# Optimization experiments

Hardware: AMD Instinct MI355X
Metric: run time of the kernel (lower is better)

The kernel has to match this reference:

```python
import jax, jax.numpy as jnp
import numpy as np
from jax import lax

N_KERNELS = 10000
IN_CH = 3
BATCH = 64
T_LEN = 1024
KSIZES = [7, 9, 11]
DILS = [1, 2, 4, 8, 16]
MAXK = max(KSIZES)

# Deterministic stand-in for torch's random per-kernel (size, dilation) draw.
_rng = np.random.default_rng(0)
_ks = np.array(KSIZES)[_rng.integers(0, len(KSIZES), N_KERNELS)]
_dil = np.array(DILS)[_rng.integers(0, len(DILS), N_KERNELS)]
GROUPS = []  # (kernel_size, dilation, static index array)
for _k in KSIZES:
    for _d in DILS:
        _idx = np.nonzero((_ks == _k) & (_dil == _d))[0]
        if _idx.size:
            GROUPS.append((_k, _d, _idx))
_PERM = np.concatenate([g[2] for g in GROUPS])  # grouped order -> original kernel id
INV_PERM = np.argsort(_PERM)                    # restore original kernel order


def setup_inputs() -> dict:
    key = jax.random.key(0)
    kx, kw, kb = jax.random.split(key, 3)
    x = jax.random.normal(kx, (BATCH, IN_CH, T_LEN), dtype=jnp.float32)
    # Weights padded to MAXK taps; taps beyond each kernel's size are zeroed
    # (zero taps do not change the conv output within the valid window).
    w = jax.random.normal(kw, (N_KERNELS, IN_CH, MAXK), dtype=jnp.float32)
    tap_mask = (np.arange(MAXK)[None, :] < _ks[:, None]).astype(np.float32)
    weights = w * jnp.asarray(tap_mask)[:, None, :]
    biases = 0.1 * jax.random.normal(kb, (N_KERNELS,), dtype=jnp.float32)
    return {"x": x, "weights": weights, "biases": biases}


def _rocket(x, weights, biases):
    # Group kernels by (size, dilation) -> <=15 batched convs instead of 10000 tiny ones.
    maxs, ppvs = [], []
    for k, d, idx in GROUPS:
        w = weights[idx, :, :k]                 # (G, C, k), idx is a static np array
        pad = (k - 1) * d // 2                  # 'same' padding (k odd -> exact)
        out = lax.conv_general_dilated(
            x, w, window_strides=(1,), padding=[(pad, pad)],
            rhs_dilation=(d,), dimension_numbers=("NCH", "OIH", "NCH"))
        out = out + biases[idx][None, :, None]  # (B, G, T)
        maxs.append(out.max(-1))                             # max pooling feature
        ppvs.append((out > 0).astype(jnp.float32).mean(-1))  # PPV feature
    mx = jnp.concatenate(maxs, 1)[:, INV_PERM]  # (B, N) in original kernel order
    pv = jnp.concatenate(ppvs, 1)[:, INV_PERM]
    # Interleave [max_0, ppv_0, max_1, ppv_1, ...] like torch.stack(features, dim=1)
    return jnp.stack([mx, pv], -1).reshape(x.shape[0], 2 * N_KERNELS)


def reference(x, weights, biases):
    return _rocket(x, weights, biases)
```

## Files before the change

### kernel.cpp

```cpp
#include <hip/hip_runtime.h>
#include <stdint.h>

#define N_KERNELS 10000
#define NCHUNK 56
#define CH_ALLOC 1312
#define PP_STRIDE (3 * CH_ALLOC)
#define NPHASE 4

typedef unsigned __int128 u128;
typedef __attribute__((ext_vector_type(4)))  short short4v;
typedef __attribute__((ext_vector_type(8)))  short short8;
typedef __attribute__((ext_vector_type(16))) float floatx16;

struct KDraws { uint8_t k[N_KERNELS]; uint8_t d[N_KERNELS]; };

constexpr KDraws make_kd() {
    KDraws kd{};
    const u128 MULT = (((u128)0x2360ED051FC65DA4ULL) << 64) | 0x4385DF649FCCF645ULL;

    uint32_t hc = 0x43b0d7e5u;
    uint32_t pool[4] = {};
    for (int i = 0; i < 4; i++) {
        uint32_t v = 0u;
        v ^= hc; hc *= 0x931e8875u;
        v *= hc; v ^= v >> 16;
        pool[i] = v;
    }
    for (int s = 0; s < 4; s++)
        for (int dd = 0; dd < 4; dd++)
            if (s != dd) {
                uint32_t hv = pool[s];
                hv ^= hc; hc *= 0x931e8875u;
                hv *= hc; hv ^= hv >> 16;
                uint32_t rr = 0xca01f9ddu * pool[dd] - 0x4973f715u * hv;
                rr ^= rr >> 16;
                pool[dd] = rr;
            }
    uint32_t st[8] = {};
    uint32_t hcb = 0x8b51f9ddu;
    for (int i = 0; i < 8; i++) {
        uint32_t dv = pool[i & 3];
        dv ^= hcb; hcb *= 0x58f38dedu;
        dv *= hcb; dv ^= dv >> 16;
        st[i] = dv;
    }
    uint64_t w0 = (uint64_t)st[0] | ((uint64_t)st[1] << 32);
    uint64_t w1 = (uint64_t)st[2] | ((uint64_t)st[3] << 32);
    uint64_t w2 = (uint64_t)st[4] | ((uint64_t)st[5] << 32);
    uint64_t w3 = (uint64_t)st[6] | ((uint64_t)st[7] << 32);
    u128 initstate = (((u128)w0) << 64) | w1;
    u128 initseq   = (((u128)w2) << 64) | w3;

    u128 inc   = (initseq << 1) | 1;
    u128 state = 0;
    state = state * MULT + inc;
    state += initstate;
    state = state * MULT + inc;

    u128 s = state;
    for (int t = 0; t < 10000; ++t) {
        s = s * MULT + inc;
        uint64_t hi = (uint64_t)(s >> 64), lo = (uint64_t)s;
        unsigned rot = (unsigned)(hi >> 58);
        uint64_t v = hi ^ lo;
        uint64_t o = (v >> rot) | (v << ((64u - rot) & 63u));
        uint32_t d0 = (uint32_t)o;
        uint32_t d1 = (uint32_t)(o >> 32);
        int i0 = 2 * t, i1 = 2 * t + 1;
        if (i0 < 10000) kd.k[i0] = (uint8_t)(((uint64_t)d0 * 3u) >> 32);
        else            kd.d[i0 - 10000] = (uint8_t)(((uint64_t)d0 * 5u) >> 32);
        if (i1 < 10000) kd.k[i1] = (uint8_t)(((uint64_t)d1 * 3u) >> 32);
        else            kd.d[i1 - 10000] = (uint8_t)(((uint64_t)d1 * 5u) >> 32);
    }
    return kd;
}

constexpr KDraws kdr = make_kd();

struct Tables {
    alignas(16) int sched[4 * NCHUNK];
    int list[N_KERNELS];
};

constexpr Tables make_tables(const KDraws& kd) {
    Tables T{};
    int cnt[15] = {}, off[15] = {}, cur[15] = {};
    for (int i = 0; i < 10000; ++i) cnt[(int)kd.k[i] * 5 + (int)kd.d[i]]++;
    int o = 0;
    for (int g = 0; g < 15; ++g) { off[g] = o; cur[g] = o; o += cnt[g]; }
    for (int i = 0; i < 10000; ++i) {
        int g = (int)kd.k[i] * 5 + (int)kd.d[i];
        T.list[cur[g]++] = i;
    }
    const int kv[3] = {7, 9, 11};
    int ci = 0;
    for (int g = 0; g < 15; ++g) {
        int sz = cnt[g];
        for (int s2 = 0; s2 < sz; s2 += 256) {
            T.sched[4 * ci + 0] = kv[g / 5];
            T.sched[4 * ci + 1] = g % 5;
            T.sched[4 * ci + 2] = off[g] + s2;
            T.sched[4 * ci + 3] = (sz - s2 < 256) ? (sz - s2) : 256;
            ci++;
        }
    }
    for (; ci < NCHUNK; ci++) {
        T.sched[4 * ci + 0] = 0; T.sched[4 * ci + 1] = 0;
        T.sched[4 * ci + 2] = 0; T.sched[4 * ci + 3] = 0;
    }
    return T;
}

__constant__ Tables g_T = make_tables(kdr);

__device__ __forceinline__ uint16_t f32_to_bf16(float v) {
    uint32_t u = __builtin_bit_cast(uint32_t, v);
    return (uint16_t)((u + 0x7FFFu + ((u >> 16) & 1u)) >> 16);
}

__device__ __forceinline__ void stat16(const floatx16& C, float& mx, int& cnt) {
    float g0 = fmaxf(fmaxf(C[0],  C[1]),  C[2]);
    float g1 = fmaxf(fmaxf(C[3],  C[4]),  C[5]);
    float g2 = fmaxf(fmaxf(C[6],  C[7]),  C[8]);
    float g3 = fmaxf(fmaxf(C[9],  C[10]), C[11]);
    float g4 = fmaxf(fmaxf(C[12], C[13]), C[14]);
    float h0 = fmaxf(fmaxf(g0, g1), g2);
    float h1 = fmaxf(fmaxf(g3, g4), C[15]);
    mx = fmaxf(mx, fmaxf(h0, h1));
    #pragma unroll
    for (int i = 0; i < 16; i += 2) {
        int s0 = __builtin_bit_cast(int, C[i])     >> 31;
        int s1 = __builtin_bit_cast(int, C[i + 1]) >> 31;
        cnt += s0 + s1;
    }
}

__device__ __forceinline__ int swz_g(int g) { return g ^ ((g >> 4) & 3); }

template <int K, int D>
__device__ __forceinline__ void body(const float* __restrict__ x,
                                     const float* __restrict__ wgt,
                                     const float* __restrict__ bias,
                                     int lstart, int valid,
                                     float* __restrict__ out,
                                     short* __restrict__ xs,
                                     int b) {
    constexpr int H   = (K - 1) / 2;
    constexpr int Q   = 1024 / D;
    constexpr int S   = Q + 16;
    constexpr int RS  = (D <= 4) ? 8 : (D == 8 ? 4 : 2);
    constexpr int NIT = 32;

    const int tid   = threadIdx.x;
    const int lane  = tid & 63;
    const int wave  = tid >> 6;
    const int jbase = (lane >> 5) * 8;
    const int m31   = lane & 31;

    for (int idx = tid; idx < 3 * (CH_ALLOC + NPHASE); idx += 256) {
        int c = idx / (CH_ALLOC + NPHASE);
        int P = idx - c * (CH_ALLOC + NPHASE);
        float v = 0.f;
        int y = P - 8;
        if (y >= 0) {
            int r = y / S;
            int q = y - r * S;
            if (r < D && q < Q) v = x[((size_t)b * 3 + c) * 1024 + r + D * q];
        }
        short hv = (short)f32_to_bf16(v);
        #pragma unroll
        for (int pp = 0; pp < NPHASE; ++pp) {
            int ee = P - pp;
            if (ee >= 0 && ee < CH_ALLOC) {
                int phys = (swz_g(ee >> 2) << 2) | (ee & 3);
                xs[pp * PP_STRIDE + c * CH_ALLOC + phys] = hv;
            }
        }
    }

    int i0 = wave * 64 + m31;
    int i1 = i0 + 32;
    int n0 = g_T.list[lstart + (i0 < valid ? i0 : valid - 1)];
    int n1 = g_T.list[lstart + (i1 < valid ? i1 : valid - 1)];
    short8 whi[2][3];
    #pragma unroll
    for (int t2 = 0; t2 < 2; ++t2) {
        int n = t2 ? n1 : n0;
        #pragma unroll
        for (int c = 0; c < 3; ++c) {
            #pragma unroll
            for (int u = 0; u < 8; ++u) {
                int j = jbase + u;
                float wv = (j < 11) ? wgt[n * 33 + c * 11 + j] : 0.f;
                whi[t2][c][u] = (short)f32_to_bf16(wv);
            }
        }
    }
    float bv0 = bias[n0], bv1 = bias[n1];

    floatx16 BT0, BT1;
    #pragma unroll
    for (int i = 0; i < 16; ++i) { BT0[i] = bv0; BT1[i] = bv1; }

    __syncthreads();

    auto calcF = [&](int it) -> int {
        int ri, p;
        if (D <= 4)      { ri = it >> 3; p = it & 7; }
        else if (D == 8) { ri = it >> 2; p = it & 3; }
        else             { ri = it >> 1; p = it & 1; }
        int q0;
        if (D == 1)      q0 = 8 + ri * 256;
        else if (D == 2) q0 = 8 + (ri >> 1) * S + (ri & 1) * 256;
        else             q0 = 8 + ri * S;
        return q0 + p - H + RS * m31;
    };
    auto loadfrag = [&](int F, short8& A0, short8& A1, short8& A2) {
        int g0 = (F >> 2) + (jbase >> 2);
        int s0 = swz_g(g0) << 2;
        int s1 = swz_g(g0 + 1) << 2;
        const short* bp = xs + (F & 3) * PP_STRIDE;
        short4v l0 = *reinterpret_cast<const short4v*>(bp + s0);
        short4v h0 = *reinterpret_cast<const short4v*>(bp + s1);
        short4v l1 = *reinterpret_cast<const short4v*>(bp + CH_ALLOC + s0);
        short4v h1 = *reinterpret_cast<const short4v*>(bp + CH_ALLOC + s1);
        short4v l2 = *reinterpret_cast<const short4v*>(bp + 2 * CH_ALLOC + s0);
        short4v h2 = *reinterpret_cast<const short4v*>(bp + 2 * CH_ALLOC + s1);
        A0 = __builtin_shufflevector(l0, h0, 0, 1, 2, 3, 4, 5, 6, 7);
        A1 = __builtin_shufflevector(l1, h1, 0, 1, 2, 3, 4, 5, 6, 7);
        A2 = __builtin_shufflevector(l2, h2, 0, 1, 2, 3, 4, 5, 6, 7);
    };

    float mx0 = -3.402823466e38f, mx1 = -3.402823466e38f;
    int cnt0 = 0, cnt1 = 0;

    short8 a0, a1, a2, b0, b1, b2;
    loadfrag(calcF(0), a0, a1, a2);
    loadfrag(calcF(1), b0, b1, b2);

    #pragma unroll 1
    for (int it = 0; it < NIT; it += 2) {
        int itA = (it + 2 < NIT) ? it + 2 : NIT - 1;
        int itB = (it + 3 < NIT) ? it + 3 : NIT - 1;

        floatx16 C0, C1;
        C0 = __builtin_amdgcn_mfma_f32_32x32x16_bf16(a0, whi[0][0], BT0, 0, 0, 0);
        C0 = __builtin_amdgcn_mfma_f32_32x32x16_bf16(a1, whi[0][1], C0, 0, 0, 0);
        C0 = __builtin_amdgcn_mfma_f32_32x32x16_bf16(a2, whi[0][2], C0, 0, 0, 0);
        C1 = __builtin_amdgcn_mfma_f32_32x32x16_bf16(a0, whi[1][0], BT1, 0, 0, 0);
        C1 = __builtin_amdgcn_mfma_f32_32x32x16_bf16(a1, whi[1][1], C1, 0, 0, 0);
        C1 = __builtin_amdgcn_mfma_f32_32x32x16_bf16(a2, whi[1][2], C1, 0, 0, 0);
        loadfrag(calcF(itA), a0, a1, a2);
        stat16(C0, mx0, cnt0);
        stat16(C1, mx1, cnt1);

        floatx16 D0, D1;
        D0 = __builtin_amdgcn_mfma_f32_32x32x16_bf16(b0, whi[0][0], BT0, 0, 0, 0);
        D0 = __builtin_amdgcn_mfma_f32_32x32x16_bf16(b1, whi[0][1], D0, 0, 0, 0);
        D0 = __builtin_amdgcn_mfma_f32_32x32x16_bf16(b2, whi[0][2], D0, 0, 0, 0);
        D1 = __builtin_amdgcn_mfma_f32_32x32x16_bf16(b0, whi[1][0], BT1, 0, 0, 0);
        D1 = __builtin_amdgcn_mfma_f32_32x32x16_bf16(b1, whi[1][1], D1, 0, 0, 0);
        D1 = __builtin_amdgcn_mfma_f32_32x32x16_bf16(b2, whi[1][2], D1, 0, 0, 0);
        loadfrag(calcF(itB), b0, b1, b2);
        stat16(D0, mx0, cnt0);
        stat16(D1, mx1, cnt1);
    }

    mx0  = fmaxf(mx0, __shfl_xor(mx0, 32));
    mx1  = fmaxf(mx1, __shfl_xor(mx1, 32));
    cnt0 += __shfl_xor(cnt0, 32);
    cnt1 += __shfl_xor(cnt1, 32);

    if (lane < 32) {
        float2* ob = reinterpret_cast<float2*>(out + (size_t)b * (2 * N_KERNELS));
        ob[n0] = make_float2(mx0, (float)(1024 + cnt0) * (1.0f / 1024.0f));
        ob[n1] = make_float2(mx1, (float)(1024 + cnt1) * (1.0f / 1024.0f));
    }
}

__global__ __launch_bounds__(256, 4)
void rocket_main(const float* __restrict__ x, const float* __restrict__ wgt,
                 const float* __restrict__ bias, float* __restrict__ out) {
    __shared__ __align__(16) short xs[NPHASE * PP_STRIDE];
    int kc     = g_T.sched[4 * blockIdx.x + 0];
    int ld2    = g_T.sched[4 * blockIdx.x + 1];
    int lstart = g_T.sched[4 * blockIdx.x + 2];
    int valid  = g_T.sched[4 * blockIdx.x + 3];
    if (valid == 0) return;
    int b = blockIdx.y;
    switch (kc * 8 + ld2) {
        case 7*8+0:  body<7, 1 >(x, wgt, bias, lstart, valid, out, xs, b); break;
        case 7*8+1:  body<7, 2 >(x, wgt, bias, lstart, valid, out, xs, b); break;
        case 7*8+2:  body<7, 4 >(x, wgt, bias, lstart, valid, out, xs, b); break;
        case 7*8+3:  body<7, 8 >(x, wgt, bias, lstart, valid, out, xs, b); break;
        case 7*8+4:  body<7, 16>(x, wgt, bias, lstart, valid, out, xs, b); break;
        case 9*8+0:  body<9, 1 >(x, wgt, bias, lstart, valid, out, xs, b); break;
        case 9*8+1:  body<9, 2 >(x, wgt, bias, lstart, valid, out, xs, b); break;
        case 9*8+2:  body<9, 4 >(x, wgt, bias, lstart, valid, out, xs, b); break;
        case 9*8+3:  body<9, 8 >(x, wgt, bias, lstart, valid, out, xs, b); break;
        case 9*8+4:  body<9, 16>(x, wgt, bias, lstart, valid, out, xs, b); break;
        case 11*8+0: body<11,1 >(x, wgt, bias, lstart, valid, out, xs, b); break;
        case 11*8+1: body<11,2 >(x, wgt, bias, lstart, valid, out, xs, b); break;
        case 11*8+2: body<11,4 >(x, wgt, bias, lstart, valid, out, xs, b); break;
        case 11*8+3: body<11,8 >(x, wgt, bias, lstart, valid, out, xs, b); break;
        default:     body<11,16>(x, wgt, bias, lstart, valid, out, xs, b); break;
    }
}

extern "C" void kernel_launch(void* const* d_in, const int* in_sizes, int n_in,
                              void* d_out, int out_size, void* d_ws, size_t ws_size,
                              hipStream_t stream) {
    const float* x   = (const float*)d_in[0];
    const float* w   = (const float*)d_in[1];
    const float* b   = (const float*)d_in[2];
    float* out = (float*)d_out;
    (void)d_ws; (void)ws_size;

    hipLaunchKernelGGL(rocket_main, dim3(NCHUNK, 64), dim3(256), 0, stream,
                       x, w, b, out);
}
```

Measured before the change: 143.1 us.

## Replace 4-phase LDS copies with register window and shift-based fragment build

Shared-memory staging now keeps a single bf16 copy of each channel instead of four phase-shifted swizzled copies. Each lane loads a 20-element window per channel once per row block and builds the eight shifted MFMA A fragments in registers with 16-bit shifts. The bias is no longer fed as the MFMA accumulator: it is added to the max at the end and used as a compare threshold for the positive count. This cuts LDS footprint and LDS traffic (which may raise occupancy) at the cost of extra VALU shift/or work and more registers for the window.

```diff
diff --git a/kernel.cpp b/kernel.cpp
--- a/kernel.cpp
+++ b/kernel.cpp
@@ -4,13 +4,12 @@
 #define N_KERNELS 10000
 #define NCHUNK 56
 #define CH_ALLOC 1312
-#define PP_STRIDE (3 * CH_ALLOC)
-#define NPHASE 4
 
 typedef unsigned __int128 u128;
-typedef __attribute__((ext_vector_type(4)))  short short4v;
 typedef __attribute__((ext_vector_type(8)))  short short8;
 typedef __attribute__((ext_vector_type(16))) float floatx16;
+typedef __attribute__((ext_vector_type(4)))  unsigned int uint4v;
+typedef __attribute__((ext_vector_type(2)))  unsigned int uint2v;
 
 struct KDraws { uint8_t k[N_KERNELS]; uint8_t d[N_KERNELS]; };
 
@@ -118,7 +117,8 @@
     return (uint16_t)((u + 0x7FFFu + ((u >> 16) & 1u)) >> 16);
 }
 
-__device__ __forceinline__ void stat16(const floatx16& C, float& mx, int& cnt) {
+__device__ __forceinline__ void stat16t(const floatx16& C, float& mx, int& cnt,
+                                        float nb) {
     float g0 = fmaxf(fmaxf(C[0],  C[1]),  C[2]);
     float g1 = fmaxf(fmaxf(C[3],  C[4]),  C[5]);
     float g2 = fmaxf(fmaxf(C[6],  C[7]),  C[8]);
@@ -128,14 +128,9 @@
     float h1 = fmaxf(fmaxf(g3, g4), C[15]);
     mx = fmaxf(mx, fmaxf(h0, h1));
     #pragma unroll
-    for (int i = 0; i < 16; i += 2) {
-        int s0 = __builtin_bit_cast(int, C[i])     >> 31;
-        int s1 = __builtin_bit_cast(int, C[i + 1]) >> 31;
-        cnt += s0 + s1;
-    }
-}
-
-__device__ __forceinline__ int swz_g(int g) { return g ^ ((g >> 4) & 3); }
+    for (int i = 0; i < 16; ++i)
+        cnt += (C[i] > nb) ? 1 : 0;
+}
 
 template <int K, int D>
 __device__ __forceinline__ void body(const float* __restrict__ x,
@@ -145,11 +140,10 @@
                                      float* __restrict__ out,
                                      short* __restrict__ xs,
                                      int b) {
-    constexpr int H   = (K - 1) / 2;
-    constexpr int Q   = 1024 / D;
-    constexpr int S   = Q + 16;
-    constexpr int RS  = (D <= 4) ? 8 : (D == 8 ? 4 : 2);
-    constexpr int NIT = 32;
+    constexpr int H = (K - 1) / 2;
+    constexpr int Q = 1024 / D;
+    constexpr int S = Q + 16;
+    constexpr int O = (8 - H) & 7;
 
     const int tid   = threadIdx.x;
     const int lane  = tid & 63;
@@ -157,9 +151,9 @@
     const int jbase = (lane >> 5) * 8;
     const int m31   = lane & 31;
 
-    for (int idx = tid; idx < 3 * (CH_ALLOC + NPHASE); idx += 256) {
-        int c = idx / (CH_ALLOC + NPHASE);
-        int P = idx - c * (CH_ALLOC + NPHASE);
+    for (int idx = tid; idx < 3 * CH_ALLOC; idx += 256) {
+        int c = idx / CH_ALLOC;
+        int P = idx - c * CH_ALLOC;
         float v = 0.f;
         int y = P - 8;
         if (y >= 0) {
@@ -167,15 +161,7 @@
             int q = y - r * S;
             if (r < D && q < Q) v = x[((size_t)b * 3 + c) * 1024 + r + D * q];
         }
-        short hv = (short)f32_to_bf16(v);
-        #pragma unroll
-        for (int pp = 0; pp < NPHASE; ++pp) {
-            int ee = P - pp;
-            if (ee >= 0 && ee < CH_ALLOC) {
-                int phys = (swz_g(ee >> 2) << 2) | (ee & 3);
-                xs[pp * PP_STRIDE + c * CH_ALLOC + phys] = hv;
-            }
-        }
+        xs[idx] = (short)f32_to_bf16(v);
     }
 
     int i0 = wave * 64 + m31;
@@ -197,73 +183,68 @@
         }
     }
     float bv0 = bias[n0], bv1 = bias[n1];
-
-    floatx16 BT0, BT1;
-    #pragma unroll
-    for (int i = 0; i < 16; ++i) { BT0[i] = bv0; BT1[i] = bv1; }
+    float nb0 = -bv0, nb1 = -bv1;
+
+    const floatx16 Zv = (floatx16)0.0f;
 
     __syncthreads();
-
-    auto calcF = [&](int it) -> int {
-        int ri, p;
-        if (D <= 4)      { ri = it >> 3; p = it & 7; }
-        else if (D == 8) { ri = it >> 2; p = it & 3; }
-        else             { ri = it >> 1; p = it & 1; }
-        int q0;
-        if (D == 1)      q0 = 8 + ri * 256;
-        else if (D == 2) q0 = 8 + (ri >> 1) * S + (ri & 1) * 256;
-        else             q0 = 8 + ri * S;
-        return q0 + p - H + RS * m31;
-    };
-    auto loadfrag = [&](int F, short8& A0, short8& A1, short8& A2) {
-        int g0 = (F >> 2) + (jbase >> 2);
-        int s0 = swz_g(g0) << 2;
-        int s1 = swz_g(g0 + 1) << 2;
-        const short* bp = xs + (F & 3) * PP_STRIDE;
-        short4v l0 = *reinterpret_cast<const short4v*>(bp + s0);
-        short4v h0 = *reinterpret_cast<const short4v*>(bp + s1);
-        short4v l1 = *reinterpret_cast<const short4v*>(bp + CH_ALLOC + s0);
-        short4v h1 = *reinterpret_cast<const short4v*>(bp + CH_ALLOC + s1);
-        short4v l2 = *reinterpret_cast<const short4v*>(bp + 2 * CH_ALLOC + s0);
-        short4v h2 = *reinterpret_cast<const short4v*>(bp + 2 * CH_ALLOC + s1);
-        A0 = __builtin_shufflevector(l0, h0, 0, 1, 2, 3, 4, 5, 6, 7);
-        A1 = __builtin_shufflevector(l1, h1, 0, 1, 2, 3, 4, 5, 6, 7);
-        A2 = __builtin_shufflevector(l2, h2, 0, 1, 2, 3, 4, 5, 6, 7);
-    };
 
     float mx0 = -3.402823466e38f, mx1 = -3.402823466e38f;
     int cnt0 = 0, cnt1 = 0;
 
-    short8 a0, a1, a2, b0, b1, b2;
-    loadfrag(calcF(0), a0, a1, a2);
-    loadfrag(calcF(1), b0, b1, b2);
-
     #pragma unroll 1
-    for (int it = 0; it < NIT; it += 2) {
-        int itA = (it + 2 < NIT) ? it + 2 : NIT - 1;
-        int itB = (it + 3 < NIT) ? it + 3 : NIT - 1;
-
-        floatx16 C0, C1;
-        C0 = __builtin_amdgcn_mfma_f32_32x32x16_bf16(a0, whi[0][0], BT0, 0, 0, 0);
-        C0 = __builtin_amdgcn_mfma_f32_32x32x16_bf16(a1, whi[0][1], C0, 0, 0, 0);
-        C0 = __builtin_amdgcn_mfma_f32_32x32x16_bf16(a2, whi[0][2], C0, 0, 0, 0);
-        C1 = __builtin_amdgcn_mfma_f32_32x32x16_bf16(a0, whi[1][0], BT1, 0, 0, 0);
-        C1 = __builtin_amdgcn_mfma_f32_32x32x16_bf16(a1, whi[1][1], C1, 0, 0, 0);
-        C1 = __builtin_amdgcn_mfma_f32_32x32x16_bf16(a2, whi[1][2], C1, 0, 0, 0);
-        loadfrag(calcF(itA), a0, a1, a2);
-        stat16(C0, mx0, cnt0);
-        stat16(C1, mx1, cnt1);
-
-        floatx16 D0, D1;
-        D0 = __builtin_amdgcn_mfma_f32_32x32x16_bf16(b0, whi[0][0], BT0, 0, 0, 0);
-        D0 = __builtin_amdgcn_mfma_f32_32x32x16_bf16(b1, whi[0][1], D0, 0, 0, 0);
-        D0 = __builtin_amdgcn_mfma_f32_32x32x16_bf16(b2, whi[0][2], D0, 0, 0, 0);
-        D1 = __builtin_amdgcn_mfma_f32_32x32x16_bf16(b0, whi[1][0], BT1, 0, 0, 0);
-        D1 = __builtin_amdgcn_mfma_f32_32x32x16_bf16(b1, whi[1][1], D1, 0, 0, 0);
-        D1 = __builtin_amdgcn_mfma_f32_32x32x16_bf16(b2, whi[1][2], D1, 0, 0, 0);
-        loadfrag(calcF(itB), b0, b1, b2);
-        stat16(D0, mx0, cnt0);
-        stat16(D1, mx1, cnt1);
+    for (int ri = 0; ri < 4; ++ri) {
+        int rb, qb;
+        if constexpr (D == 1)      { rb = 0;                   qb = 256 * ri + 8 * m31; }
+        else if constexpr (D == 2) { rb = ri >> 1;             qb = (ri & 1) * 256 + 8 * m31; }
+        else if constexpr (D == 4) { rb = ri;                  qb = 8 * m31; }
+        else if constexpr (D == 8) { rb = 2 * ri + (m31 >> 4); qb = 8 * (m31 & 15); }
+        else                       { rb = 4 * ri + (m31 >> 3); qb = 8 * (m31 & 7); }
+        int Bm    = 8 - H + rb * S + qb;
+        int rbase = (Bm - O) + jbase;
+
+        uint32_t w[3][10];
+        #pragma unroll
+        for (int c = 0; c < 3; ++c) {
+            const short* bp = xs + c * CH_ALLOC + rbase;
+            uint4v u0 = *reinterpret_cast<const uint4v*>(bp);
+            uint4v u1 = *reinterpret_cast<const uint4v*>(bp + 8);
+            uint2v u2 = *reinterpret_cast<const uint2v*>(bp + 16);
+            w[c][0] = u0[0]; w[c][1] = u0[1]; w[c][2] = u0[2]; w[c][3] = u0[3];
+            w[c][4] = u1[0]; w[c][5] = u1[1]; w[c][6] = u1[2]; w[c][7] = u1[3];
+            w[c][8] = u2[0]; w[c][9] = u2[1];
+        }
+
+        #pragma unroll
+        for (int p = 0; p < 8; ++p) {
+            const int s = O + p;
+            const int j = s >> 1;
+            short8 A0, A1, A2;
+            #pragma unroll
+            for (int c = 0; c < 3; ++c) {
+                uint4v t;
+                if (s & 1) {
+                    t[0] = (w[c][j]     >> 16) | (w[c][j + 1] << 16);
+                    t[1] = (w[c][j + 1] >> 16) | (w[c][j + 2] << 16);
+                    t[2] = (w[c][j + 2] >> 16) | (w[c][j + 3] << 16);
+                    t[3] = (w[c][j + 3] >> 16) | (w[c][j + 4] << 16);
+                } else {
+                    t[0] = w[c][j];     t[1] = w[c][j + 1];
+                    t[2] = w[c][j + 2]; t[3] = w[c][j + 3];
+                }
+                short8 Ac = __builtin_bit_cast(short8, t);
+                if (c == 0) A0 = Ac; else if (c == 1) A1 = Ac; else A2 = Ac;
+            }
+            floatx16 C0, C1;
+            C0 = __builtin_amdgcn_mfma_f32_32x32x16_bf16(A0, whi[0][0], Zv, 0, 0, 0);
+            C1 = __builtin_amdgcn_mfma_f32_32x32x16_bf16(A0, whi[1][0], Zv, 0, 0, 0);
+            C0 = __builtin_amdgcn_mfma_f32_32x32x16_bf16(A1, whi[0][1], C0, 0, 0, 0);
+            C1 = __builtin_amdgcn_mfma_f32_32x32x16_bf16(A1, whi[1][1], C1, 0, 0, 0);
+            C0 = __builtin_amdgcn_mfma_f32_32x32x16_bf16(A2, whi[0][2], C0, 0, 0, 0);
+            C1 = __builtin_amdgcn_mfma_f32_32x32x16_bf16(A2, whi[1][2], C1, 0, 0, 0);
+            stat16t(C0, mx0, cnt0, nb0);
+            stat16t(C1, mx1, cnt1, nb1);
+        }
     }
 
     mx0  = fmaxf(mx0, __shfl_xor(mx0, 32));
@@ -273,15 +254,15 @@
 
     if (lane < 32) {
         float2* ob = reinterpret_cast<float2*>(out + (size_t)b * (2 * N_KERNELS));
-        ob[n0] = make_float2(mx0, (float)(1024 + cnt0) * (1.0f / 1024.0f));
-        ob[n1] = make_float2(mx1, (float)(1024 + cnt1) * (1.0f / 1024.0f));
+        ob[n0] = make_float2(mx0 + bv0, (float)cnt0 * (1.0f / 1024.0f));
+        ob[n1] = make_float2(mx1 + bv1, (float)cnt1 * (1.0f / 1024.0f));
     }
 }
 
 __global__ __launch_bounds__(256, 4)
 void rocket_main(const float* __restrict__ x, const float* __restrict__ wgt,
                  const float* __restrict__ bias, float* __restrict__ out) {
-    __shared__ __align__(16) short xs[NPHASE * PP_STRIDE];
+    __shared__ __align__(16) short xs[3 * CH_ALLOC];
     int kc     = g_T.sched[4 * blockIdx.x + 0];
     int ld2    = g_T.sched[4 * blockIdx.x + 1];
     int lstart = g_T.sched[4 * blockIdx.x + 2];
```

Result: slower. 156.8 us (+9.6%).

## Fold bias into MFMA, skew accumulator pipeline, launch only real chunks

Applied to the files above, without the earlier changes.

Puts the bias into the unused 16th weight tap, paired with a constant-one input lane, so the MFMAs start from a zero accumulator instead of a broadcast bias tile. This frees accumulator registers and drops the bias setup. The main loop is restructured into a skewed even/odd schedule: MFMAs for one pair of kernels interleave with statistics on the previous results, with prologue and epilogue iterations added. The grid is also sized to the exact number of scheduled chunks rather than padded NCHUNK, which skips empty blocks. Bias is now rounded to bf16, which slightly changes precision.

```diff
diff --git a/kernel.cpp b/kernel.cpp
--- a/kernel.cpp
+++ b/kernel.cpp
@@ -113,6 +113,16 @@
 
 __constant__ Tables g_T = make_tables(kdr);
 
+constexpr int count_chunks() {
+    int cnt[15] = {};
+    for (int i = 0; i < 10000; ++i) cnt[(int)kdr.k[i] * 5 + (int)kdr.d[i]]++;
+    int ci = 0;
+    for (int g = 0; g < 15; ++g)
+        for (int s2 = 0; s2 < cnt[g]; s2 += 256) ci++;
+    return ci;
+}
+constexpr int NCHUNK_REAL = count_chunks();
+
 __device__ __forceinline__ uint16_t f32_to_bf16(float v) {
     uint32_t u = __builtin_bit_cast(uint32_t, v);
     return (uint16_t)((u + 0x7FFFu + ((u >> 16) & 1u)) >> 16);
@@ -156,6 +166,7 @@
     const int wave  = tid >> 6;
     const int jbase = (lane >> 5) * 8;
     const int m31   = lane & 31;
+    const bool hi   = (jbase == 8);
 
     for (int idx = tid; idx < 3 * (CH_ALLOC + NPHASE); idx += 256) {
         int c = idx / (CH_ALLOC + NPHASE);
@@ -182,25 +193,26 @@
     int i1 = i0 + 32;
     int n0 = g_T.list[lstart + (i0 < valid ? i0 : valid - 1)];
     int n1 = g_T.list[lstart + (i1 < valid ? i1 : valid - 1)];
+    float bv0 = bias[n0], bv1 = bias[n1];
     short8 whi[2][3];
     #pragma unroll
     for (int t2 = 0; t2 < 2; ++t2) {
         int n = t2 ? n1 : n0;
+        float bv = t2 ? bv1 : bv0;
         #pragma unroll
         for (int c = 0; c < 3; ++c) {
             #pragma unroll
             for (int u = 0; u < 8; ++u) {
                 int j = jbase + u;
                 float wv = (j < 11) ? wgt[n * 33 + c * 11 + j] : 0.f;
+                if (c == 2 && u == 7 && hi) wv = bv;
                 whi[t2][c][u] = (short)f32_to_bf16(wv);
             }
         }
     }
-    float bv0 = bias[n0], bv1 = bias[n1];
-
-    floatx16 BT0, BT1;
-    #pragma unroll
-    for (int i = 0; i < 16; ++i) { BT0[i] = bv0; BT1[i] = bv1; }
+
+    const floatx16 Zv = (floatx16)0.0f;
+    const short one_bf16 = (short)0x3F80;
 
     __syncthreads();
 
@@ -215,7 +227,8 @@
         else             q0 = 8 + ri * S;
         return q0 + p - H + RS * m31;
     };
-    auto loadfrag = [&](int F, short8& A0, short8& A1, short8& A2) {
+    short8 F0, F1, F2;
+    auto loadfrag = [&](int F) {
         int g0 = (F >> 2) + (jbase >> 2);
         int s0 = swz_g(g0) << 2;
         int s1 = swz_g(g0 + 1) << 2;
@@ -226,45 +239,59 @@
         short4v h1 = *reinterpret_cast<const short4v*>(bp + CH_ALLOC + s1);
         short4v l2 = *reinterpret_cast<const short4v*>(bp + 2 * CH_ALLOC + s0);
         short4v h2 = *reinterpret_cast<const short4v*>(bp + 2 * CH_ALLOC + s1);
-        A0 = __builtin_shufflevector(l0, h0, 0, 1, 2, 3, 4, 5, 6, 7);
-        A1 = __builtin_shufflevector(l1, h1, 0, 1, 2, 3, 4, 5, 6, 7);
-        A2 = __builtin_shufflevector(l2, h2, 0, 1, 2, 3, 4, 5, 6, 7);
+        F0 = __builtin_shufflevector(l0, h0, 0, 1, 2, 3, 4, 5, 6, 7);
+        F1 = __builtin_shufflevector(l1, h1, 0, 1, 2, 3, 4, 5, 6, 7);
+        F2 = __builtin_shufflevector(l2, h2, 0, 1, 2, 3, 4, 5, 6, 7);
+        F2[7] = hi ? one_bf16 : F2[7];
     };
 
     float mx0 = -3.402823466e38f, mx1 = -3.402823466e38f;
     int cnt0 = 0, cnt1 = 0;
 
-    short8 a0, a1, a2, b0, b1, b2;
-    loadfrag(calcF(0), a0, a1, a2);
-    loadfrag(calcF(1), b0, b1, b2);
+    floatx16 E0, E1, O0, O1;
+
+    loadfrag(calcF(0));
+    E0 = __builtin_amdgcn_mfma_f32_32x32x16_bf16(F0, whi[0][0], Zv, 0, 0, 0);
+    E1 = __builtin_amdgcn_mfma_f32_32x32x16_bf16(F0, whi[1][0], Zv, 0, 0, 0);
+    E0 = __builtin_amdgcn_mfma_f32_32x32x16_bf16(F1, whi[0][1], E0, 0, 0, 0);
+    E1 = __builtin_amdgcn_mfma_f32_32x32x16_bf16(F1, whi[1][1], E1, 0, 0, 0);
+    E0 = __builtin_amdgcn_mfma_f32_32x32x16_bf16(F2, whi[0][2], E0, 0, 0, 0);
+    E1 = __builtin_amdgcn_mfma_f32_32x32x16_bf16(F2, whi[1][2], E1, 0, 0, 0);
+    loadfrag(calcF(1));
+    stat16(E1, mx1, cnt1);
 
     #pragma unroll 1
-    for (int it = 0; it < NIT; it += 2) {
-        int itA = (it + 2 < NIT) ? it + 2 : NIT - 1;
-        int itB = (it + 3 < NIT) ? it + 3 : NIT - 1;
-
-        floatx16 C0, C1;
-        C0 = __builtin_amdgcn_mfma_f32_32x32x16_bf16(a0, whi[0][0], BT0, 0, 0, 0);
-        C0 = __builtin_amdgcn_mfma_f32_32x32x16_bf16(a1, whi[0][1], C0, 0, 0, 0);
-        C0 = __builtin_amdgcn_mfma_f32_32x32x16_bf16(a2, whi[0][2], C0, 0, 0, 0);
-        C1 = __builtin_amdgcn_mfma_f32_32x32x16_bf16(a0, whi[1][0], BT1, 0, 0, 0);
-        C1 = __builtin_amdgcn_mfma_f32_32x32x16_bf16(a1, whi[1][1], C1, 0, 0, 0);
-        C1 = __builtin_amdgcn_mfma_f32_32x32x16_bf16(a2, whi[1][2], C1, 0, 0, 0);
-        loadfrag(calcF(itA), a0, a1, a2);
-        stat16(C0, mx0, cnt0);
-        stat16(C1, mx1, cnt1);
-
-        floatx16 D0, D1;
-        D0 = __builtin_amdgcn_mfma_f32_32x32x16_bf16(b0, whi[0][0], BT0, 0, 0, 0);
-        D0 = __builtin_amdgcn_mfma_f32_32x32x16_bf16(b1, whi[0][1], D0, 0, 0, 0);
-        D0 = __builtin_amdgcn_mfma_f32_32x32x16_bf16(b2, whi[0][2], D0, 0, 0, 0);
-        D1 = __builtin_amdgcn_mfma_f32_32x32x16_bf16(b0, whi[1][0], BT1, 0, 0, 0);
-        D1 = __builtin_amdgcn_mfma_f32_32x32x16_bf16(b1, whi[1][1], D1, 0, 0, 0);
-        D1 = __builtin_amdgcn_mfma_f32_32x32x16_bf16(b2, whi[1][2], D1, 0, 0, 0);
-        loadfrag(calcF(itB), b0, b1, b2);
-        stat16(D0, mx0, cnt0);
-        stat16(D1, mx1, cnt1);
-    }
+    for (int it = 1; it < NIT - 1; it += 2) {
+        O0 = __builtin_amdgcn_mfma_f32_32x32x16_bf16(F0, whi[0][0], Zv, 0, 0, 0);
+        O1 = __builtin_amdgcn_mfma_f32_32x32x16_bf16(F0, whi[1][0], Zv, 0, 0, 0);
+        O0 = __builtin_amdgcn_mfma_f32_32x32x16_bf16(F1, whi[0][1], O0, 0, 0, 0);
+        O1 = __builtin_amdgcn_mfma_f32_32x32x16_bf16(F1, whi[1][1], O1, 0, 0, 0);
+        O0 = __builtin_amdgcn_mfma_f32_32x32x16_bf16(F2, whi[0][2], O0, 0, 0, 0);
+        O1 = __builtin_amdgcn_mfma_f32_32x32x16_bf16(F2, whi[1][2], O1, 0, 0, 0);
+        loadfrag(calcF(it + 1));
+        stat16(E0, mx0, cnt0);
+        stat16(O1, mx1, cnt1);
+
+        E0 = __builtin_amdgcn_mfma_f32_32x32x16_bf16(F0, whi[0][0], Zv, 0, 0, 0);
+        E1 = __builtin_amdgcn_mfma_f32_32x32x16_bf16(F0, whi[1][0], Zv, 0, 0, 0);
+        E0 = __builtin_amdgcn_mfma_f32_32x32x16_bf16(F1, whi[0][1], E0, 0, 0, 0);
+        E1 = __builtin_amdgcn_mfma_f32_32x32x16_bf16(F1, whi[1][1], E1, 0, 0, 0);
+        E0 = __builtin_amdgcn_mfma_f32_32x32x16_bf16(F2, whi[0][2], E0, 0, 0, 0);
+        E1 = __builtin_amdgcn_mfma_f32_32x32x16_bf16(F2, whi[1][2], E1, 0, 0, 0);
+        loadfrag(calcF(it + 2));
+        stat16(O0, mx0, cnt0);
+        stat16(E1, mx1, cnt1);
+    }
+
+    O0 = __builtin_amdgcn_mfma_f32_32x32x16_bf16(F0, whi[0][0], Zv, 0, 0, 0);
+    O1 = __builtin_amdgcn_mfma_f32_32x32x16_bf16(F0, whi[1][0], Zv, 0, 0, 0);
+    O0 = __builtin_amdgcn_mfma_f32_32x32x16_bf16(F1, whi[0][1], O0, 0, 0, 0);
+    O1 = __builtin_amdgcn_mfma_f32_32x32x16_bf16(F1, whi[1][1], O1, 0, 0, 0);
+    O0 = __builtin_amdgcn_mfma_f32_32x32x16_bf16(F2, whi[0][2], O0, 0, 0, 0);
+    O1 = __builtin_amdgcn_mfma_f32_32x32x16_bf16(F2, whi[1][2], O1, 0, 0, 0);
+    stat16(E0, mx0, cnt0);
+    stat16(O1, mx1, cnt1);
+    stat16(O0, mx0, cnt0);
 
     mx0  = fmaxf(mx0, __shfl_xor(mx0, 32));
     mx1  = fmaxf(mx1, __shfl_xor(mx1, 32));
@@ -316,6 +343,6 @@
     float* out = (float*)d_out;
     (void)d_ws; (void)ws_size;
 
-    hipLaunchKernelGGL(rocket_main, dim3(NCHUNK, 64), dim3(256), 0, stream,
+    hipLaunchKernelGGL(rocket_main, dim3(NCHUNK_REAL, 64), dim3(256), 0, stream,
                        x, w, b, out);
 }
```

New measurement: 136.3 us. -4.7%, faster.
